# Optimization experiments

Measured on AMD Instinct MI355X. Metric: run time of the kernel, lower is better.

## Reference

```python
import jax, jax.numpy as jnp
import numpy as np

B, L, D = 32, 256, 1024
H = 8
DQ = D // H            # 128, dim_q == dim_k
DS = 64                # dim_s
DM = 256               # dim_mlp_s
DF = 4096              # dim_feedforward
EPS = 1e-5


def _layernorm(x, g, b):
    mu = jnp.mean(x, axis=-1, keepdims=True)
    var = jnp.mean(jnp.square(x - mu), axis=-1, keepdims=True)
    return (x - mu) * jax.lax.rsqrt(var + EPS) * g + b


def setup_inputs() -> dict:
    key = jax.random.key(0)
    ks = jax.random.split(key, 20)
    s = 0.02
    inp = {
        'src': jax.random.normal(ks[0], (B, L, D), jnp.float32),
        'sf': jax.random.normal(ks[1], (B, DS), jnp.float32),
        'atten_mask': jax.random.randint(ks[2], (B, L, L), 0, 2, jnp.int32),
        # per-head projections, stacked over heads (in,out layout)
        'qw': jax.random.normal(ks[3], (H, D, DQ), jnp.float32) * s,
        'qb': jnp.zeros((H, DQ), jnp.float32),
        'kw': jax.random.normal(ks[4], (H, D, DQ), jnp.float32) * s,
        'kb': jnp.zeros((H, DQ), jnp.float32),
        'vw': jax.random.normal(ks[5], (H, D, DQ), jnp.float32) * s,
        'vb': jnp.zeros((H, DQ), jnp.float32),
        # per-head bias MLP: dim_s -> dim_mlp_s -> L*L
        'b1w': jax.random.normal(ks[6], (H, DS, DM), jnp.float32) * s,
        'b1b': jnp.zeros((H, DM), jnp.float32),
        'b2w': jax.random.normal(ks[7], (H, DM, L * L), jnp.float32) * s,
        'b2b': jnp.zeros((H, L * L), jnp.float32),
        # output projection
        'ow': jax.random.normal(ks[8], (H * DQ, D), jnp.float32) * s,
        'ob': jnp.zeros((D,), jnp.float32),
        # layernorms
        'ln1_g': jnp.ones((D,), jnp.float32), 'ln1_b': jnp.zeros((D,), jnp.float32),
        'ln2_g': jnp.ones((D,), jnp.float32), 'ln2_b': jnp.zeros((D,), jnp.float32),
        # feed-forward
        'w1': jax.random.normal(ks[9], (D, DF), jnp.float32) * s,
        'bf1': jnp.zeros((DF,), jnp.float32),
        'w2': jax.random.normal(ks[10], (DF, D), jnp.float32) * s,
        'bf2': jnp.zeros((D,), jnp.float32),
    }
    return inp


def reference(src, sf, atten_mask, qw, qb, kw, kb, vw, vb, b1w, b1b, b2w, b2b,
              ow, ob, ln1_g, ln1_b, ln2_g, ln2_b, w1, bf1, w2, bf2):
    mask = atten_mask.astype(bool)                      # (B,L,L)
    # per-head projections: (H,B,L,DQ)
    q = jnp.einsum('bld,hdq->hblq', src, qw) + qb[:, None, None, :]
    k = jnp.einsum('bld,hdq->hblq', src, kw) + kb[:, None, None, :]
    v = jnp.einsum('bld,hdq->hblq', src, vw) + vb[:, None, None, :]
    scale = q.shape[-1] ** 0.5
    scores = jnp.einsum('hblq,hbmq->hblm', q, k) / scale
    # masked_fill with constant 1e-9 (NOT -inf), as in the original
    scores = jnp.where(mask[None], jnp.float32(1e-9), scores)
    # per-head learned bias from side features, added AFTER softmax
    hid = jax.nn.relu(jnp.einsum('bs,hsm->hbm', sf, b1w) + b1b[:, None, :])
    bias = (jnp.einsum('hbm,hmn->hbn', hid, b2w) + b2b[:, None, :]).reshape(H, B, L, L)
    soft = jax.nn.softmax(scores, axis=-1) + bias
    out = jnp.einsum('hblm,hbmv->hblv', soft, v)        # (H,B,L,DQ)
    # faithful to original: each head's result is indexed [0] -> batch element 0
    head0 = out[:, 0]                                   # (H,L,DQ)
    hidden = jnp.transpose(head0, (1, 0, 2)).reshape(L, H * DQ)
    attn = hidden @ ow + ob                             # (L,D), broadcasts over batch
    x = _layernorm(src + attn[None], ln1_g, ln1_b)      # (B,L,D)
    ffn = jax.nn.relu(x @ w1 + bf1) @ w2 + bf2
    return _layernorm(x + ffn, ln2_g, ln2_b)
```

## Files before the change

kernel.cpp:

```cpp
#include <hip/hip_runtime.h>

typedef unsigned short u16;
typedef short s16x8 __attribute__((ext_vector_type(8)));
typedef u16 u16x4 __attribute__((ext_vector_type(4)));
typedef float f32x4 __attribute__((ext_vector_type(4)));

#define B_ 32
#define L_ 256
#define D_ 1024
#define H_ 8
#define DQ_ 128
#define DS_ 64
#define DM_ 256
#define DF_ 4096

__device__ __forceinline__ u16 f2bf(float f) {
  unsigned u = __float_as_uint(f);
  unsigned r = (u + 0x7FFFu + ((u >> 16) & 1u)) >> 16;
  return (u16)r;
}
__device__ __forceinline__ float bf2f(u16 x) {
  return __uint_as_float(((unsigned)x) << 16);
}

__device__ __forceinline__ f32x4 mfma16(s16x8 a, s16x8 b, f32x4 c) {
  return __builtin_amdgcn_mfma_f32_16x16x32_bf16(a, b, c, 0, 0, 0);
}

#define GLDS16(g, l)                                                        \
  __builtin_amdgcn_global_load_lds(                                         \
      (__attribute__((address_space(1))) const void*)(g),                   \
      (__attribute__((address_space(3))) void*)(l), 16, 0, 0)

__device__ __forceinline__ void tile_tr(const float* __restrict__ ip,
                                        u16* __restrict__ op, int K, int N,
                                        int bx, int by, float (*t)[33], int tid) {
  const int tx = tid & 31, ty = tid >> 5;
  const long n0 = (long)bx * 32, k0 = (long)by * 32;
#pragma unroll
  for (int i = 0; i < 4; ++i)
    t[ty + i * 8][tx] = ip[(k0 + ty + i * 8) * (long)N + n0 + tx];
  __syncthreads();
#pragma unroll
  for (int i = 0; i < 4; ++i)
    op[(n0 + ty + i * 8) * (long)K + k0 + tx] = f2bf(t[tx][ty + i * 8]);
}

__global__ __launch_bounds__(256) void prep(
    const float* __restrict__ qw, const float* __restrict__ kw,
    const float* __restrict__ vw, const float* __restrict__ ow,
    const float* __restrict__ w1, const float* __restrict__ w2,
    const float* __restrict__ src, const float* __restrict__ sf,
    const float* __restrict__ b1w, const float* __restrict__ b1b,
    u16* __restrict__ qwT, u16* __restrict__ kwT, u16* __restrict__ vwT,
    u16* __restrict__ owT, u16* __restrict__ w1T, u16* __restrict__ w2T,
    u16* __restrict__ src0b, float* __restrict__ nzv, int* __restrict__ nzi,
    int* __restrict__ nzcnt) {
  const int b = blockIdx.x;
  const int tid = threadIdx.x;
  __shared__ float t[32][33];
  __shared__ float s_sf[DS_];
  __shared__ int wcnt[4];
  if (b < 3072) {
    const int z = b >> 7, rem = b & 127;
    const int sel = z >> 3, h = z & 7;
    const float* ip = (sel == 0 ? qw : (sel == 1 ? kw : vw)) + (long)h * D_ * DQ_;
    u16* op = (sel == 0 ? qwT : (sel == 1 ? kwT : vwT)) + (long)h * DQ_ * D_;
    tile_tr(ip, op, D_, DQ_, rem & 3, rem >> 2, t, tid);
  } else if (b < 4096) {
    const int rem = b - 3072;
    tile_tr(ow, owT, D_, D_, rem & 31, rem >> 5, t, tid);
  } else if (b < 8192) {
    const int rem = b - 4096;
    tile_tr(w1, w1T, D_, DF_, rem & 127, rem >> 7, t, tid);
  } else if (b < 12288) {
    const int rem = b - 8192;
    tile_tr(w2, w2T, DF_, D_, rem & 31, rem >> 5, t, tid);
  } else if (b < 12544) {
    const int rem = b - 12288;
    const int i = (rem * 256 + tid) * 4;
    float4 v = *(const float4*)(src + i);
    u16x4 o = {f2bf(v.x), f2bf(v.y), f2bf(v.z), f2bf(v.w)};
    *(u16x4*)(src0b + i) = o;
  } else {
    const int h = b - 12544;
    if (tid < DS_) s_sf[tid] = sf[tid];
    __syncthreads();
    float a = b1b[h * DM_ + tid];
    const float* wp = b1w + (long)h * DS_ * DM_ + tid;
#pragma unroll 8
    for (int s = 0; s < DS_; ++s) a += s_sf[s] * wp[s * DM_];
    a = fmaxf(a, 0.f);
    const unsigned long long bal = __ballot(a > 0.f);
    const int lane = tid & 63, wv = tid >> 6;
    const int pc = __popcll(bal);
    if (lane == 0) wcnt[wv] = pc;
    __syncthreads();
    int base = 0;
    for (int i = 0; i < wv; ++i) base += wcnt[i];
    const int pos = base + __popcll(bal & ((1ull << lane) - 1ull));
    if (a > 0.f) { nzv[h * DM_ + pos] = a; nzi[h * DM_ + pos] = tid; }
    if (tid == 255) nzcnt[h] = base + pc;
  }
}

__global__ __launch_bounds__(256) void phase2(
    const float* __restrict__ nzv, const int* __restrict__ nzi,
    const int* __restrict__ nzcnt, const float* __restrict__ b2w,
    const float* __restrict__ b2b, float* __restrict__ biasb,
    const u16* __restrict__ src0b, const u16* __restrict__ qwT,
    const u16* __restrict__ kwT, const u16* __restrict__ vwT,
    const float* __restrict__ qb, const float* __restrict__ kb,
    const float* __restrict__ vb, u16* __restrict__ q0, u16* __restrict__ k0,
    u16* __restrict__ v0T) {
  const int b = blockIdx.x;
  const int tid = threadIdx.x;
  __shared__ float sv[DM_];
  __shared__ int si[DM_];
  __shared__ u16 smA[128 * 32];
  __shared__ u16 smB[128 * 32];
  if (b < 512) {
    const int h = b >> 6;
    const int n0 = (b & 63) << 10;
    const int nnz = nzcnt[h];
    if (tid < DM_) { sv[tid] = nzv[h * DM_ + tid]; si[tid] = nzi[h * DM_ + tid]; }
    __syncthreads();
    const float* wb = b2w + (long)h * DM_ * 65536 + n0 + tid * 4;
    float4 acc = {0.f, 0.f, 0.f, 0.f};
    int j = 0;
    for (; j + 4 <= nnz; j += 4) {
      const float4 a0 = *(const float4*)(wb + (long)si[j] * 65536);
      const float4 a1 = *(const float4*)(wb + (long)si[j + 1] * 65536);
      const float4 a2 = *(const float4*)(wb + (long)si[j + 2] * 65536);
      const float4 a3 = *(const float4*)(wb + (long)si[j + 3] * 65536);
      const float v0 = sv[j], v1 = sv[j + 1], v2 = sv[j + 2], v3 = sv[j + 3];
      acc.x += v0 * a0.x + v1 * a1.x + v2 * a2.x + v3 * a3.x;
      acc.y += v0 * a0.y + v1 * a1.y + v2 * a2.y + v3 * a3.y;
      acc.z += v0 * a0.z + v1 * a1.z + v2 * a2.z + v3 * a3.z;
      acc.w += v0 * a0.w + v1 * a1.w + v2 * a2.w + v3 * a3.w;
    }
    for (; j < nnz; ++j) {
      const float4 a0 = *(const float4*)(wb + (long)si[j] * 65536);
      const float v0 = sv[j];
      acc.x += v0 * a0.x; acc.y += v0 * a0.y; acc.z += v0 * a0.z; acc.w += v0 * a0.w;
    }
    const float4 bb = *(const float4*)(b2b + (long)h * 65536 + n0 + tid * 4);
    float4 o = {acc.x + bb.x, acc.y + bb.y, acc.z + bb.z, acc.w + bb.w};
    *(float4*)(biasb + (long)h * 65536 + n0 + tid * 4) = o;
  } else {
    const int r = b - 512;
    const int z = r >> 1, sel = z >> 3, h = z & 7;
    const long tm = (long)(r & 1) * 128;
    const int K = D_;
    const u16* BT = (sel == 0 ? qwT : (sel == 1 ? kwT : vwT)) + (long)h * DQ_ * D_;
    const float* bias = (sel == 0 ? qb : (sel == 1 ? kb : vb)) + h * DQ_;
    const int lane = tid & 63;
    const int wv = tid >> 6;
    const int wr = wv >> 1, wc = wv & 1;
    const u16* ga = src0b + (tm + (tid >> 2)) * (long)K + (tid & 3) * 8;
    const u16* gb = BT + (long)(tid >> 2) * K + (tid & 3) * 8;
    const long rstep = 64L * K;
    u16* la = &smA[tid * 8];
    u16* lb = &smB[tid * 8];
    f32x4 acc[4][4];
#pragma unroll
    for (int m = 0; m < 4; ++m)
#pragma unroll
      for (int n = 0; n < 4; ++n) acc[m][n] = (f32x4){0.f, 0.f, 0.f, 0.f};
    for (int k0_ = 0; k0_ < K; k0_ += 32) {
      GLDS16(ga + k0_, la);
      GLDS16(ga + rstep + k0_, la + 64 * 32);
      GLDS16(gb + k0_, lb);
      GLDS16(gb + rstep + k0_, lb + 64 * 32);
      __syncthreads();
      s16x8 af[4], bf[4];
      const int ka = (lane >> 4) * 8;
      const int ra = wr * 64 + (lane & 15);
      const int rb = wc * 64 + (lane & 15);
#pragma unroll
      for (int m = 0; m < 4; ++m) af[m] = *(const s16x8*)&smA[(ra + m * 16) * 32 + ka];
#pragma unroll
      for (int n = 0; n < 4; ++n) bf[n] = *(const s16x8*)&smB[(rb + n * 16) * 32 + ka];
#pragma unroll
      for (int m = 0; m < 4; ++m)
#pragma unroll
        for (int n = 0; n < 4; ++n) acc[m][n] = mfma16(af[m], bf[n], acc[m][n]);
      __syncthreads();
    }
    const long crow0 = tm + wr * 64 + ((lane >> 4) * 4);
    const long ccol0 = wc * 64 + (lane & 15);
#pragma unroll
    for (int m = 0; m < 4; ++m) {
#pragma unroll
      for (int n = 0; n < 4; ++n) {
#pragma unroll
        for (int i = 0; i < 4; ++i) {
          const long row = crow0 + m * 16 + i;
          const long col = ccol0 + n * 16;
          const float v = acc[m][n][i] + bias[col];
          if (sel < 2) {
            u16* o = (sel == 0 ? q0 : k0) + (long)h * L_ * DQ_;
            o[row * DQ_ + col] = f2bf(v);
          } else {
            v0T[(long)h * DQ_ * L_ + col * L_ + row] = f2bf(v);
          }
        }
      }
    }
  }
}

__global__ __launch_bounds__(256) void gemm_bt(
    const u16* __restrict__ A, const u16* __restrict__ BT, float* __restrict__ C,
    const float* __restrict__ bias, int K, int ldc) {
  __shared__ u16 smA[128 * 32];
  __shared__ u16 smB[128 * 32];
  const int tid = threadIdx.x;
  const int lane = tid & 63;
  const int wv = tid >> 6;
  const int wr = wv >> 1, wc = wv & 1;
  const long tm = (long)blockIdx.x * 128;
  const long tn = (long)blockIdx.y * 128;

  const u16* ga = A + (tm + (tid >> 2)) * (long)K + (tid & 3) * 8;
  const u16* gb = BT + (tn + (tid >> 2)) * (long)K + (tid & 3) * 8;
  const long rstep = 64L * K;
  u16* la = &smA[tid * 8];
  u16* lb = &smB[tid * 8];

  f32x4 acc[4][4];
#pragma unroll
  for (int m = 0; m < 4; ++m)
#pragma unroll
    for (int n = 0; n < 4; ++n) acc[m][n] = (f32x4){0.f, 0.f, 0.f, 0.f};

  for (int k0 = 0; k0 < K; k0 += 32) {
    GLDS16(ga + k0, la);
    GLDS16(ga + rstep + k0, la + 64 * 32);
    GLDS16(gb + k0, lb);
    GLDS16(gb + rstep + k0, lb + 64 * 32);
    __syncthreads();
    s16x8 af[4], bf[4];
    const int ka = (lane >> 4) * 8;
    const int ra = wr * 64 + (lane & 15);
    const int rb = wc * 64 + (lane & 15);
#pragma unroll
    for (int m = 0; m < 4; ++m) af[m] = *(const s16x8*)&smA[(ra + m * 16) * 32 + ka];
#pragma unroll
    for (int n = 0; n < 4; ++n) bf[n] = *(const s16x8*)&smB[(rb + n * 16) * 32 + ka];
#pragma unroll
    for (int m = 0; m < 4; ++m)
#pragma unroll
      for (int n = 0; n < 4; ++n) acc[m][n] = mfma16(af[m], bf[n], acc[m][n]);
    __syncthreads();
  }

  const long crow0 = tm + wr * 64 + ((lane >> 4) * 4);
  const long ccol0 = tn + wc * 64 + (lane & 15);
#pragma unroll
  for (int m = 0; m < 4; ++m)
#pragma unroll
    for (int n = 0; n < 4; ++n)
#pragma unroll
      for (int i = 0; i < 4; ++i) {
        const long row = crow0 + m * 16 + i;
        const long col = ccol0 + n * 16;
        C[row * (long)ldc + col] = acc[m][n][i] + bias[col];
      }
}

template <int BN, int EPI>
__global__ __launch_bounds__(512, 2) void gemm8p(
    const u16* __restrict__ A, const u16* __restrict__ BT, void* __restrict__ Cv,
    const float* __restrict__ bias, const void* __restrict__ R, int M, int N,
    int K, int ldc) {
  extern __shared__ char lds[];
  constexpr int NR = BN / 64;
  constexpr int NHB = BN / 128;
  constexpr int BUF = 32768 + BN * 128;
  constexpr int WST = (NHB == 2) ? 4 : 2;
  const int tid = threadIdx.x;
  const int lane = tid & 63;
  const int w = tid >> 6;
  const int wr = w >> 2, wc = w & 3;

  const int total = gridDim.x;
  int bid = blockIdx.x;
  int s = ((total & 7) == 0) ? ((bid & 7) * (total >> 3) + (bid >> 3)) : bid;
  const int gn = N / BN;
  const long tm = (long)(s / gn) * 256;
  const long tn = (long)(s % gn) * BN;
  const int NT = K >> 6;

  auto stageA = [&](int half, int t) {
    char* hb = lds + (long)(t & 1) * BUF + half * 16384;
    const u16* g = A + (tm + half * 128) * (long)K + (long)t * 64;
#pragma unroll
    for (int j = 0; j < 2; ++j) {
      const int idx = j * 512 + tid;
      const int r = idx >> 3;
      const int c16 = (idx & 7) ^ (r & 7);
      GLDS16(g + (long)r * K + c16 * 8, hb + idx * 16);
    }
  };
  auto stageB = [&](int half, int t) {
    char* hb = lds + (long)(t & 1) * BUF + 32768 + half * 16384;
    const u16* g = BT + (tn + half * 128) * (long)K + (long)t * 64;
#pragma unroll
    for (int j = 0; j < 2; ++j) {
      const int idx = j * 512 + tid;
      const int r = idx >> 3;
      const int c16 = (idx & 7) ^ (r & 7);
      GLDS16(g + (long)r * K + c16 * 8, hb + idx * 16);
    }
  };

  stageA(0, 0);
  stageA(1, 0);
  stageB(0, 0);
  if (NHB == 2) stageB(1, 0);
  stageB(0, 1);
  if (NHB == 2) stageB(1, 1);
  asm volatile("s_waitcnt vmcnt(%0)" ::"n"(WST) : "memory");
  __builtin_amdgcn_s_barrier();

  f32x4 acc[8][NR];
#pragma unroll
  for (int m = 0; m < 8; ++m)
#pragma unroll
    for (int n = 0; n < NR; ++n) acc[m][n] = (f32x4){0.f, 0.f, 0.f, 0.f};

  const int lk = (lane >> 4) * 16;
  const int lr = lane & 15;

  for (int t = 0; t < NT; ++t) {
    const char* bp = lds + (long)(t & 1) * BUF;
    s16x8 bfr[NR][2];
#pragma unroll
    for (int p = 0; p < 4; ++p) {
      if (p == 0) {
#pragma unroll
        for (int ni = 0; ni < NR; ++ni) {
          const int brow = wc * (BN / 4) + ni * 16 + lr;
#pragma unroll
          for (int ks = 0; ks < 2; ++ks) {
            const int kb = (ks * 64 + lk) ^ ((brow & 7) << 4);
            bfr[ni][ks] = *(const s16x8*)(bp + 32768 + brow * 128 + kb);
          }
        }
      }
      s16x8 afr[2][2];
#pragma unroll
      for (int rI = 0; rI < 2; ++rI) {
        const int arow = wr * 128 + (2 * p + rI) * 16 + lr;
#pragma unroll
        for (int ks = 0; ks < 2; ++ks) {
          const int kb = (ks * 64 + lk) ^ ((arow & 7) << 4);
          afr[rI][ks] = *(const s16x8*)(bp + arow * 128 + kb);
        }
      }
      if (p == 0) {
        if (t + 1 < NT) stageA(0, t + 1);
      } else if (p == 1) {
        if (t + 1 < NT) stageA(1, t + 1);
      } else if (p == 2) {
        if (t + 2 < NT) stageB(0, t + 2);
      } else {
        if (NHB == 2 && t + 2 < NT) stageB(1, t + 2);
      }
      __builtin_amdgcn_s_barrier();
      __builtin_amdgcn_s_setprio(1);
#pragma unroll
      for (int rI = 0; rI < 2; ++rI)
#pragma unroll
        for (int ni = 0; ni < NR; ++ni)
#pragma unroll
          for (int ks = 0; ks < 2; ++ks)
            acc[2 * p + rI][ni] = mfma16(afr[rI][ks], bfr[ni][ks], acc[2 * p + rI][ni]);
      __builtin_amdgcn_s_setprio(0);
      if (p == 3) {
        if (t + 2 < NT) {
          asm volatile("s_waitcnt vmcnt(%0)" ::"n"(WST) : "memory");
        } else if (t + 1 < NT) {
          asm volatile("s_waitcnt vmcnt(0)" ::: "memory");
        }
      }
      __builtin_amdgcn_s_barrier();
    }
  }

  const long crow0 = tm + wr * 128 + ((lane >> 4) * 4);
  const long ccol0 = tn + wc * (BN / 4) + lr;
#pragma unroll
  for (int m = 0; m < 8; ++m) {
#pragma unroll
    for (int n = 0; n < NR; ++n) {
#pragma unroll
      for (int i = 0; i < 4; ++i) {
        const long row = crow0 + m * 16 + i;
        const long col = ccol0 + n * 16;
        const float v = acc[m][n][i] + bias[col];
        if constexpr (EPI == 1) {
          ((u16*)Cv)[row * (long)ldc + col] = f2bf(fmaxf(v, 0.f));
        } else {
          const float r = bf2f(((const u16*)R)[row * (long)ldc + col]);
          ((u16*)Cv)[row * (long)ldc + col] = f2bf(v + r);
        }
      }
    }
  }
}

__global__ __launch_bounds__(64) void attn_kernel(
    const u16* __restrict__ q0, const u16* __restrict__ k0,
    const u16* __restrict__ vT, const float* __restrict__ biasb,
    const int* __restrict__ mask0, u16* __restrict__ hidden) {
  const int lane = threadIdx.x;
  const int h = blockIdx.y;
  const int r0 = blockIdx.x * 16;
  const u16* q = q0 + (long)h * L_ * DQ_;
  const u16* k = k0 + (long)h * L_ * DQ_;
  const u16* v = vT + (long)h * DQ_ * L_;
  const int lg = lane >> 4;
  const int ll = lane & 15;

  s16x8 aq[4];
#pragma unroll
  for (int kk = 0; kk < 4; ++kk)
    aq[kk] = *(const s16x8*)(q + (long)(r0 + ll) * DQ_ + kk * 32 + lg * 8);

  float sc[16][4];
  const float scale = 0.08838834764831845f;
#pragma unroll
  for (int t = 0; t < 16; ++t) {
    f32x4 a = {0.f, 0.f, 0.f, 0.f};
#pragma unroll
    for (int kk = 0; kk < 4; ++kk) {
      s16x8 bf = *(const s16x8*)(k + (long)(t * 16 + ll) * DQ_ + kk * 32 + lg * 8);
      a = mfma16(aq[kk], bf, a);
    }
#pragma unroll
    for (int i = 0; i < 4; ++i) {
      const int row = r0 + lg * 4 + i;
      const int col = t * 16 + ll;
      float s = a[i] * scale;
      if (mask0[row * L_ + col] != 0) s = 1e-9f;
      sc[t][i] = s;
    }
  }
#pragma unroll
  for (int i = 0; i < 4; ++i) {
    float mx = sc[0][i];
#pragma unroll
    for (int t = 1; t < 16; ++t) mx = fmaxf(mx, sc[t][i]);
#pragma unroll
    for (int d = 1; d < 16; d <<= 1) mx = fmaxf(mx, __shfl_xor(mx, d));
    float sum = 0.f;
#pragma unroll
    for (int t = 0; t < 16; ++t) {
      const float e = __expf(sc[t][i] - mx);
      sc[t][i] = e;
      sum += e;
    }
#pragma unroll
    for (int d = 1; d < 16; d <<= 1) sum += __shfl_xor(sum, d);
    const float inv = 1.f / sum;
    const int row = r0 + lg * 4 + i;
#pragma unroll
    for (int t = 0; t < 16; ++t)
      sc[t][i] = sc[t][i] * inv + biasb[(long)h * 65536 + (long)row * 256 + t * 16 + ll];
  }
  __shared__ float sm[16 * 256];
#pragma unroll
  for (int t = 0; t < 16; ++t)
#pragma unroll
    for (int i = 0; i < 4; ++i)
      sm[(lg * 4 + i) * 256 + t * 16 + ll] = sc[t][i];
  __syncthreads();
  s16x8 af[8];
#pragma unroll
  for (int kk = 0; kk < 8; ++kk) {
    const float* ap = &sm[ll * 256 + kk * 32 + lg * 8];
    s16x8 t8;
#pragma unroll
    for (int j = 0; j < 8; ++j) t8[j] = (short)f2bf(ap[j]);
    af[kk] = t8;
  }
#pragma unroll
  for (int n = 0; n < 8; ++n) {
    f32x4 a = {0.f, 0.f, 0.f, 0.f};
#pragma unroll
    for (int kk = 0; kk < 8; ++kk) {
      s16x8 bf = *(const s16x8*)(v + (long)(n * 16 + ll) * 256 + kk * 32 + lg * 8);
      a = mfma16(af[kk], bf, a);
    }
#pragma unroll
    for (int i = 0; i < 4; ++i) {
      const int row = r0 + lg * 4 + i;
      const int col = n * 16 + ll;
      hidden[(long)row * 1024 + h * 128 + col] = f2bf(a[i]);
    }
  }
}

template <int MODE>
__global__ __launch_bounds__(256) void ln_kernel(
    const void* __restrict__ in0v, const float* __restrict__ add1,
    const float* __restrict__ g, const float* __restrict__ bb,
    void* __restrict__ outv) {
  const int tid = threadIdx.x;
  const long row = blockIdx.x;
  float4 v;
  if constexpr (MODE == 0) {
    v = ((const float4*)((const float*)in0v + row * D_))[tid];
    const float4 u = ((const float4*)(add1 + (row & (L_ - 1)) * D_))[tid];
    v.x += u.x; v.y += u.y; v.z += u.z; v.w += u.w;
  } else {
    const uint2 pk = *(const uint2*)((const u16*)in0v + row * D_ + tid * 4);
    v.x = __uint_as_float((pk.x & 0xFFFFu) << 16);
    v.y = __uint_as_float(pk.x & 0xFFFF0000u);
    v.z = __uint_as_float((pk.y & 0xFFFFu) << 16);
    v.w = __uint_as_float(pk.y & 0xFFFF0000u);
  }
  float s = v.x + v.y + v.z + v.w;
  float q = v.x * v.x + v.y * v.y + v.z * v.z + v.w * v.w;
#pragma unroll
  for (int d = 1; d < 64; d <<= 1) { s += __shfl_xor(s, d); q += __shfl_xor(q, d); }
  __shared__ float ss[4], sq[4];
  const int wv = tid >> 6;
  if ((tid & 63) == 0) { ss[wv] = s; sq[wv] = q; }
  __syncthreads();
  s = ss[0] + ss[1] + ss[2] + ss[3];
  q = sq[0] + sq[1] + sq[2] + sq[3];
  const float mu = s * (1.f / D_);
  const float var = q * (1.f / D_) - mu * mu;
  const float rs = rsqrtf(var + 1e-5f);
  const float4 gv = ((const float4*)g)[tid];
  const float4 bv = ((const float4*)bb)[tid];
  float4 o;
  o.x = (v.x - mu) * rs * gv.x + bv.x;
  o.y = (v.y - mu) * rs * gv.y + bv.y;
  o.z = (v.z - mu) * rs * gv.z + bv.z;
  o.w = (v.w - mu) * rs * gv.w + bv.w;
  if constexpr (MODE == 0) {
    uint2 pk;
    pk.x = (unsigned)f2bf(o.x) | ((unsigned)f2bf(o.y) << 16);
    pk.y = (unsigned)f2bf(o.z) | ((unsigned)f2bf(o.w) << 16);
    *(uint2*)((u16*)outv + row * D_ + tid * 4) = pk;
  } else {
    ((float4*)((float*)outv + row * D_))[tid] = o;
  }
}

extern "C" void kernel_launch(void* const* d_in, const int* in_sizes, int n_in,
                              void* d_out, int out_size, void* d_ws, size_t ws_size,
                              hipStream_t stream) {
  (void)in_sizes; (void)n_in; (void)out_size; (void)ws_size;
  const float* src = (const float*)d_in[0];
  const float* sf = (const float*)d_in[1];
  const int* mask = (const int*)d_in[2];
  const float* qw = (const float*)d_in[3];
  const float* qb = (const float*)d_in[4];
  const float* kw = (const float*)d_in[5];
  const float* kb = (const float*)d_in[6];
  const float* vw = (const float*)d_in[7];
  const float* vb = (const float*)d_in[8];
  const float* b1w = (const float*)d_in[9];
  const float* b1b = (const float*)d_in[10];
  const float* b2w = (const float*)d_in[11];
  const float* b2b = (const float*)d_in[12];
  const float* ow = (const float*)d_in[13];
  const float* ob = (const float*)d_in[14];
  const float* ln1g = (const float*)d_in[15];
  const float* ln1b = (const float*)d_in[16];
  const float* ln2g = (const float*)d_in[17];
  const float* ln2b = (const float*)d_in[18];
  const float* w1 = (const float*)d_in[19];
  const float* bf1 = (const float*)d_in[20];
  const float* w2 = (const float*)d_in[21];
  const float* bf2 = (const float*)d_in[22];
  float* out = (float*)d_out;

  char* ws = (char*)d_ws;
  size_t off = 0;
  auto alloc = [&](size_t bytes) {
    void* p = ws + off;
    off += (bytes + 255) & ~(size_t)255;
    return p;
  };
  u16* qwT = (u16*)alloc((size_t)H_ * DQ_ * D_ * 2);
  u16* kwT = (u16*)alloc((size_t)H_ * DQ_ * D_ * 2);
  u16* vwT = (u16*)alloc((size_t)H_ * DQ_ * D_ * 2);
  u16* owT = (u16*)alloc((size_t)D_ * D_ * 2);
  u16* w1T = (u16*)alloc((size_t)DF_ * D_ * 2);
  u16* w2T = (u16*)alloc((size_t)D_ * DF_ * 2);
  u16* src0b = (u16*)alloc((size_t)L_ * D_ * 2);
  u16* q0 = (u16*)alloc((size_t)H_ * L_ * DQ_ * 2);
  u16* k0 = (u16*)alloc((size_t)H_ * L_ * DQ_ * 2);
  u16* v0T = (u16*)alloc((size_t)H_ * DQ_ * L_ * 2);
  float* nzv = (float*)alloc((size_t)H_ * DM_ * 4);
  int* nzi = (int*)alloc((size_t)H_ * DM_ * 4);
  int* nzcnt = (int*)alloc(256);
  float* biasb = (float*)alloc((size_t)H_ * L_ * L_ * 4);
  u16* hidden = (u16*)alloc((size_t)L_ * H_ * DQ_ * 2);
  float* attnvec = (float*)alloc((size_t)L_ * D_ * 4);
  u16* xb = (u16*)alloc((size_t)B_ * L_ * D_ * 2);
  u16* ffnh = (u16*)alloc((size_t)B_ * L_ * DF_ * 2);
  u16* yb = (u16*)alloc((size_t)B_ * L_ * D_ * 2);

  hipFuncSetAttribute((const void*)gemm8p<256, 1>,
                      hipFuncAttributeMaxDynamicSharedMemorySize, 131072);
  hipFuncSetAttribute((const void*)gemm8p<128, 2>,
                      hipFuncAttributeMaxDynamicSharedMemorySize, 98304);

  const dim3 b256(256);
  prep<<<dim3(12552), b256, 0, stream>>>(qw, kw, vw, ow, w1, w2, src, sf, b1w, b1b,
                                         qwT, kwT, vwT, owT, w1T, w2T, src0b, nzv,
                                         nzi, nzcnt);
  phase2<<<dim3(560), b256, 0, stream>>>(nzv, nzi, nzcnt, b2w, b2b, biasb, src0b,
                                         qwT, kwT, vwT, qb, kb, vb, q0, k0, v0T);
  attn_kernel<<<dim3(16, H_), dim3(64), 0, stream>>>(q0, k0, v0T, biasb, mask, hidden);
  gemm_bt<<<dim3(2, 8), b256, 0, stream>>>(hidden, owT, attnvec, ob, D_, D_);
  ln_kernel<0><<<dim3(B_ * L_), b256, 0, stream>>>(src, attnvec, ln1g, ln1b, xb);
  gemm8p<256, 1><<<dim3(512), dim3(512), 131072, stream>>>(
      xb, w1T, ffnh, bf1, nullptr, B_ * L_, DF_, D_, DF_);
  gemm8p<128, 2><<<dim3(256), dim3(512), 98304, stream>>>(
      ffnh, w2T, yb, bf2, xb, B_ * L_, D_, DF_, D_);
  ln_kernel<1><<<dim3(B_ * L_), b256, 0, stream>>>(yb, nullptr, ln2g, ln2b, out);
}
```

Measured before the change: 329.0 us.

## Fuse mid-pipeline stages into cooperative persistent kernels with grid syncs

Replaces the separate phase2, attention, output projection and LN1 launches with one cooperative persistent kernel. It uses an atomic work queue for the bias GEMV and QKV items, then grid-wide syncs between attention, projection and LN1. The FFN2 GEMM and final LayerNorm are likewise fused into one cooperative kernel with a grid sync. This cuts launch overhead and inter-kernel bubbles, at the cost of grid.sync latency, reduced parallelism in some phases (e.g. only 16 blocks for projection), and co-residency requirements for cooperative launch.

```diff
diff --git a/kernel.cpp b/kernel.cpp
--- a/kernel.cpp
+++ b/kernel.cpp
@@ -1,4 +1,7 @@
 #include <hip/hip_runtime.h>
+#include <hip/hip_cooperative_groups.h>
+
+namespace cg = cooperative_groups;
 
 typedef unsigned short u16;
 typedef short s16x8 __attribute__((ext_vector_type(8)));
@@ -55,7 +58,7 @@
     u16* __restrict__ qwT, u16* __restrict__ kwT, u16* __restrict__ vwT,
     u16* __restrict__ owT, u16* __restrict__ w1T, u16* __restrict__ w2T,
     u16* __restrict__ src0b, float* __restrict__ nzv, int* __restrict__ nzi,
-    int* __restrict__ nzcnt) {
+    int* __restrict__ nzcnt, int* __restrict__ qhead) {
   const int b = blockIdx.x;
   const int tid = threadIdx.x;
   __shared__ float t[32][33];
@@ -84,6 +87,7 @@
     *(u16x4*)(src0b + i) = o;
   } else {
     const int h = b - 12544;
+    if (h == 0 && tid == 0) *qhead = 0;
     if (tid < DS_) s_sf[tid] = sf[tid];
     __syncthreads();
     float a = b1b[h * DM_ + tid];
@@ -104,136 +108,35 @@
   }
 }
 
-__global__ __launch_bounds__(256) void phase2(
-    const float* __restrict__ nzv, const int* __restrict__ nzi,
-    const int* __restrict__ nzcnt, const float* __restrict__ b2w,
-    const float* __restrict__ b2b, float* __restrict__ biasb,
-    const u16* __restrict__ src0b, const u16* __restrict__ qwT,
-    const u16* __restrict__ kwT, const u16* __restrict__ vwT,
-    const float* __restrict__ qb, const float* __restrict__ kb,
-    const float* __restrict__ vb, u16* __restrict__ q0, u16* __restrict__ k0,
-    u16* __restrict__ v0T) {
-  const int b = blockIdx.x;
-  const int tid = threadIdx.x;
-  __shared__ float sv[DM_];
-  __shared__ int si[DM_];
-  __shared__ u16 smA[128 * 32];
-  __shared__ u16 smB[128 * 32];
-  if (b < 512) {
-    const int h = b >> 6;
-    const int n0 = (b & 63) << 10;
-    const int nnz = nzcnt[h];
-    if (tid < DM_) { sv[tid] = nzv[h * DM_ + tid]; si[tid] = nzi[h * DM_ + tid]; }
-    __syncthreads();
-    const float* wb = b2w + (long)h * DM_ * 65536 + n0 + tid * 4;
-    float4 acc = {0.f, 0.f, 0.f, 0.f};
-    int j = 0;
-    for (; j + 4 <= nnz; j += 4) {
-      const float4 a0 = *(const float4*)(wb + (long)si[j] * 65536);
-      const float4 a1 = *(const float4*)(wb + (long)si[j + 1] * 65536);
-      const float4 a2 = *(const float4*)(wb + (long)si[j + 2] * 65536);
-      const float4 a3 = *(const float4*)(wb + (long)si[j + 3] * 65536);
-      const float v0 = sv[j], v1 = sv[j + 1], v2 = sv[j + 2], v3 = sv[j + 3];
-      acc.x += v0 * a0.x + v1 * a1.x + v2 * a2.x + v3 * a3.x;
-      acc.y += v0 * a0.y + v1 * a1.y + v2 * a2.y + v3 * a3.y;
-      acc.z += v0 * a0.z + v1 * a1.z + v2 * a2.z + v3 * a3.z;
-      acc.w += v0 * a0.w + v1 * a1.w + v2 * a2.w + v3 * a3.w;
-    }
-    for (; j < nnz; ++j) {
-      const float4 a0 = *(const float4*)(wb + (long)si[j] * 65536);
-      const float v0 = sv[j];
-      acc.x += v0 * a0.x; acc.y += v0 * a0.y; acc.z += v0 * a0.z; acc.w += v0 * a0.w;
-    }
-    const float4 bb = *(const float4*)(b2b + (long)h * 65536 + n0 + tid * 4);
-    float4 o = {acc.x + bb.x, acc.y + bb.y, acc.z + bb.z, acc.w + bb.w};
-    *(float4*)(biasb + (long)h * 65536 + n0 + tid * 4) = o;
-  } else {
-    const int r = b - 512;
-    const int z = r >> 1, sel = z >> 3, h = z & 7;
-    const long tm = (long)(r & 1) * 128;
-    const int K = D_;
-    const u16* BT = (sel == 0 ? qwT : (sel == 1 ? kwT : vwT)) + (long)h * DQ_ * D_;
-    const float* bias = (sel == 0 ? qb : (sel == 1 ? kb : vb)) + h * DQ_;
-    const int lane = tid & 63;
-    const int wv = tid >> 6;
-    const int wr = wv >> 1, wc = wv & 1;
-    const u16* ga = src0b + (tm + (tid >> 2)) * (long)K + (tid & 3) * 8;
-    const u16* gb = BT + (long)(tid >> 2) * K + (tid & 3) * 8;
-    const long rstep = 64L * K;
-    u16* la = &smA[tid * 8];
-    u16* lb = &smB[tid * 8];
-    f32x4 acc[4][4];
-#pragma unroll
-    for (int m = 0; m < 4; ++m)
-#pragma unroll
-      for (int n = 0; n < 4; ++n) acc[m][n] = (f32x4){0.f, 0.f, 0.f, 0.f};
-    for (int k0_ = 0; k0_ < K; k0_ += 32) {
-      GLDS16(ga + k0_, la);
-      GLDS16(ga + rstep + k0_, la + 64 * 32);
-      GLDS16(gb + k0_, lb);
-      GLDS16(gb + rstep + k0_, lb + 64 * 32);
-      __syncthreads();
-      s16x8 af[4], bf[4];
-      const int ka = (lane >> 4) * 8;
-      const int ra = wr * 64 + (lane & 15);
-      const int rb = wc * 64 + (lane & 15);
-#pragma unroll
-      for (int m = 0; m < 4; ++m) af[m] = *(const s16x8*)&smA[(ra + m * 16) * 32 + ka];
-#pragma unroll
-      for (int n = 0; n < 4; ++n) bf[n] = *(const s16x8*)&smB[(rb + n * 16) * 32 + ka];
-#pragma unroll
-      for (int m = 0; m < 4; ++m)
-#pragma unroll
-        for (int n = 0; n < 4; ++n) acc[m][n] = mfma16(af[m], bf[n], acc[m][n]);
-      __syncthreads();
-    }
-    const long crow0 = tm + wr * 64 + ((lane >> 4) * 4);
-    const long ccol0 = wc * 64 + (lane & 15);
-#pragma unroll
-    for (int m = 0; m < 4; ++m) {
-#pragma unroll
-      for (int n = 0; n < 4; ++n) {
-#pragma unroll
-        for (int i = 0; i < 4; ++i) {
-          const long row = crow0 + m * 16 + i;
-          const long col = ccol0 + n * 16;
-          const float v = acc[m][n][i] + bias[col];
-          if (sel < 2) {
-            u16* o = (sel == 0 ? q0 : k0) + (long)h * L_ * DQ_;
-            o[row * DQ_ + col] = f2bf(v);
-          } else {
-            v0T[(long)h * DQ_ * L_ + col * L_ + row] = f2bf(v);
-          }
-        }
-      }
-    }
-  }
-}
-
-__global__ __launch_bounds__(256) void gemm_bt(
-    const u16* __restrict__ A, const u16* __restrict__ BT, float* __restrict__ C,
-    const float* __restrict__ bias, int K, int ldc) {
-  __shared__ u16 smA[128 * 32];
-  __shared__ u16 smB[128 * 32];
+struct MidArgs {
+  const float* nzv; const int* nzi; const int* nzcnt;
+  const float* b2w; const float* b2b; float* biasb;
+  const u16* src0b; const u16* qwT; const u16* kwT; const u16* vwT;
+  const float* qb; const float* kb; const float* vb;
+  u16* q0; u16* k0; u16* v0T;
+  const int* mask; u16* hidden;
+  const u16* owT; const float* ob; float* attnvec;
+  const float* src; const float* ln1g; const float* ln1b; u16* xb;
+  int* qhead;
+};
+
+__device__ __forceinline__ void g128_core(const u16* __restrict__ A,
+                                          const u16* __restrict__ BT, int K,
+                                          u16* smA, u16* smB,
+                                          f32x4 (&acc)[4][4]) {
   const int tid = threadIdx.x;
   const int lane = tid & 63;
   const int wv = tid >> 6;
   const int wr = wv >> 1, wc = wv & 1;
-  const long tm = (long)blockIdx.x * 128;
-  const long tn = (long)blockIdx.y * 128;
-
-  const u16* ga = A + (tm + (tid >> 2)) * (long)K + (tid & 3) * 8;
-  const u16* gb = BT + (tn + (tid >> 2)) * (long)K + (tid & 3) * 8;
+  const u16* ga = A + (long)(tid >> 2) * K + (tid & 3) * 8;
+  const u16* gb = BT + (long)(tid >> 2) * K + (tid & 3) * 8;
   const long rstep = 64L * K;
   u16* la = &smA[tid * 8];
   u16* lb = &smB[tid * 8];
-
-  f32x4 acc[4][4];
 #pragma unroll
   for (int m = 0; m < 4; ++m)
 #pragma unroll
     for (int n = 0; n < 4; ++n) acc[m][n] = (f32x4){0.f, 0.f, 0.f, 0.f};
-
   for (int k0 = 0; k0 < K; k0 += 32) {
     GLDS16(ga + k0, la);
     GLDS16(ga + rstep + k0, la + 64 * 32);
@@ -254,9 +157,55 @@
       for (int n = 0; n < 4; ++n) acc[m][n] = mfma16(af[m], bf[n], acc[m][n]);
     __syncthreads();
   }
-
+}
+
+__device__ __forceinline__ void gemv_item(int item, const MidArgs& a,
+                                          float* sv, int* si) {
+  const int tid = threadIdx.x;
+  const int h = item >> 6;
+  const int n0 = (item & 63) << 10;
+  const int nnz = a.nzcnt[h];
+  sv[tid] = a.nzv[h * DM_ + tid];
+  si[tid] = a.nzi[h * DM_ + tid];
+  __syncthreads();
+  const float* wb = a.b2w + (long)h * DM_ * 65536 + n0 + tid * 4;
+  float4 acc = {0.f, 0.f, 0.f, 0.f};
+  int j = 0;
+  for (; j + 4 <= nnz; j += 4) {
+    const float4 a0 = *(const float4*)(wb + (long)si[j] * 65536);
+    const float4 a1 = *(const float4*)(wb + (long)si[j + 1] * 65536);
+    const float4 a2 = *(const float4*)(wb + (long)si[j + 2] * 65536);
+    const float4 a3 = *(const float4*)(wb + (long)si[j + 3] * 65536);
+    const float v0 = sv[j], v1 = sv[j + 1], v2 = sv[j + 2], v3 = sv[j + 3];
+    acc.x += v0 * a0.x + v1 * a1.x + v2 * a2.x + v3 * a3.x;
+    acc.y += v0 * a0.y + v1 * a1.y + v2 * a2.y + v3 * a3.y;
+    acc.z += v0 * a0.z + v1 * a1.z + v2 * a2.z + v3 * a3.z;
+    acc.w += v0 * a0.w + v1 * a1.w + v2 * a2.w + v3 * a3.w;
+  }
+  for (; j < nnz; ++j) {
+    const float4 a0 = *(const float4*)(wb + (long)si[j] * 65536);
+    const float v0 = sv[j];
+    acc.x += v0 * a0.x; acc.y += v0 * a0.y; acc.z += v0 * a0.z; acc.w += v0 * a0.w;
+  }
+  const float4 bb = *(const float4*)(a.b2b + (long)h * 65536 + n0 + tid * 4);
+  float4 o = {acc.x + bb.x, acc.y + bb.y, acc.z + bb.z, acc.w + bb.w};
+  *(float4*)(a.biasb + (long)h * 65536 + n0 + tid * 4) = o;
+}
+
+__device__ __forceinline__ void qkv_item(int r, const MidArgs& a, u16* smA,
+                                         u16* smB) {
+  const int tid = threadIdx.x;
+  const int z = r >> 1, sel = z >> 3, h = z & 7;
+  const long tm = (long)(r & 1) * 128;
+  const u16* BT = (sel == 0 ? a.qwT : (sel == 1 ? a.kwT : a.vwT)) + (long)h * DQ_ * D_;
+  const float* bias = (sel == 0 ? a.qb : (sel == 1 ? a.kb : a.vb)) + h * DQ_;
+  f32x4 acc[4][4];
+  g128_core(a.src0b + tm * D_, BT, D_, smA, smB, acc);
+  const int lane = tid & 63;
+  const int wv = tid >> 6;
+  const int wr = wv >> 1, wc = wv & 1;
   const long crow0 = tm + wr * 64 + ((lane >> 4) * 4);
-  const long ccol0 = tn + wc * 64 + (lane & 15);
+  const long ccol0 = wc * 64 + (lane & 15);
 #pragma unroll
   for (int m = 0; m < 4; ++m)
 #pragma unroll
@@ -265,25 +214,203 @@
       for (int i = 0; i < 4; ++i) {
         const long row = crow0 + m * 16 + i;
         const long col = ccol0 + n * 16;
-        C[row * (long)ldc + col] = acc[m][n][i] + bias[col];
-      }
-}
-
-template <int BN, int EPI>
-__global__ __launch_bounds__(512, 2) void gemm8p(
-    const u16* __restrict__ A, const u16* __restrict__ BT, void* __restrict__ Cv,
-    const float* __restrict__ bias, const void* __restrict__ R, int M, int N,
-    int K, int ldc) {
+        const float v = acc[m][n][i] + bias[col];
+        if (sel < 2) {
+          u16* o = (sel == 0 ? a.q0 : a.k0) + (long)h * L_ * DQ_;
+          o[row * DQ_ + col] = f2bf(v);
+        } else {
+          a.v0T[(long)h * DQ_ * L_ + col * L_ + row] = f2bf(v);
+        }
+      }
+}
+
+__device__ void attn_item(int item, const MidArgs& a, float* sm) {
+  const int tid = threadIdx.x;
+  const int h = item >> 4;
+  const int r0 = (item & 15) << 4;
+  const u16* q = a.q0 + (long)h * L_ * DQ_;
+  const u16* k = a.k0 + (long)h * L_ * DQ_;
+  const u16* v = a.v0T + (long)h * DQ_ * L_;
+  const int lg = (tid >> 4) & 3;
+  const int ll = tid & 15;
+  float sc[16][4];
+  if (tid < 64) {
+    s16x8 aq[4];
+#pragma unroll
+    for (int kk = 0; kk < 4; ++kk)
+      aq[kk] = *(const s16x8*)(q + (long)(r0 + ll) * DQ_ + kk * 32 + lg * 8);
+    const float scale = 0.08838834764831845f;
+#pragma unroll
+    for (int t = 0; t < 16; ++t) {
+      f32x4 acc = {0.f, 0.f, 0.f, 0.f};
+#pragma unroll
+      for (int kk = 0; kk < 4; ++kk) {
+        s16x8 bf = *(const s16x8*)(k + (long)(t * 16 + ll) * DQ_ + kk * 32 + lg * 8);
+        acc = mfma16(aq[kk], bf, acc);
+      }
+#pragma unroll
+      for (int i = 0; i < 4; ++i) {
+        const int row = r0 + lg * 4 + i;
+        const int col = t * 16 + ll;
+        float s = acc[i] * scale;
+        if (a.mask[row * L_ + col] != 0) s = 1e-9f;
+        sc[t][i] = s;
+      }
+    }
+#pragma unroll
+    for (int i = 0; i < 4; ++i) {
+      float mx = sc[0][i];
+#pragma unroll
+      for (int t = 1; t < 16; ++t) mx = fmaxf(mx, sc[t][i]);
+#pragma unroll
+      for (int d = 1; d < 16; d <<= 1) mx = fmaxf(mx, __shfl_xor(mx, d));
+      float sum = 0.f;
+#pragma unroll
+      for (int t = 0; t < 16; ++t) {
+        const float e = __expf(sc[t][i] - mx);
+        sc[t][i] = e;
+        sum += e;
+      }
+#pragma unroll
+      for (int d = 1; d < 16; d <<= 1) sum += __shfl_xor(sum, d);
+      const float inv = 1.f / sum;
+      const int row = r0 + lg * 4 + i;
+#pragma unroll
+      for (int t = 0; t < 16; ++t)
+        sc[t][i] = sc[t][i] * inv + a.biasb[(long)h * 65536 + (long)row * 256 + t * 16 + ll];
+    }
+#pragma unroll
+    for (int t = 0; t < 16; ++t)
+#pragma unroll
+      for (int i = 0; i < 4; ++i)
+        sm[(lg * 4 + i) * 256 + t * 16 + ll] = sc[t][i];
+  }
+  __syncthreads();
+  if (tid < 64) {
+    s16x8 af[8];
+#pragma unroll
+    for (int kk = 0; kk < 8; ++kk) {
+      const float* ap = &sm[ll * 256 + kk * 32 + lg * 8];
+      s16x8 t8;
+#pragma unroll
+      for (int j = 0; j < 8; ++j) t8[j] = (short)f2bf(ap[j]);
+      af[kk] = t8;
+    }
+#pragma unroll
+    for (int n = 0; n < 8; ++n) {
+      f32x4 acc = {0.f, 0.f, 0.f, 0.f};
+#pragma unroll
+      for (int kk = 0; kk < 8; ++kk) {
+        s16x8 bf = *(const s16x8*)(v + (long)(n * 16 + ll) * 256 + kk * 32 + lg * 8);
+        acc = mfma16(af[kk], bf, acc);
+      }
+#pragma unroll
+      for (int i = 0; i < 4; ++i) {
+        const int row = r0 + lg * 4 + i;
+        const int col = n * 16 + ll;
+        a.hidden[(long)row * 1024 + h * 128 + col] = f2bf(acc[i]);
+      }
+    }
+  }
+}
+
+__device__ __forceinline__ void proj_item(int item, const MidArgs& a, u16* smA,
+                                          u16* smB) {
+  const int tid = threadIdx.x;
+  const long tm = (long)(item >> 3) * 128;
+  const long tn = (long)(item & 7) * 128;
+  f32x4 acc[4][4];
+  g128_core(a.hidden + tm * D_, a.owT + tn * D_, D_, smA, smB, acc);
+  const int lane = tid & 63;
+  const int wv = tid >> 6;
+  const int wr = wv >> 1, wc = wv & 1;
+  const long crow0 = tm + wr * 64 + ((lane >> 4) * 4);
+  const long ccol0 = tn + wc * 64 + (lane & 15);
+#pragma unroll
+  for (int m = 0; m < 4; ++m)
+#pragma unroll
+    for (int n = 0; n < 4; ++n)
+#pragma unroll
+      for (int i = 0; i < 4; ++i) {
+        const long row = crow0 + m * 16 + i;
+        const long col = ccol0 + n * 16;
+        a.attnvec[row * (long)D_ + col] = acc[m][n][i] + a.ob[col];
+      }
+}
+
+__device__ __forceinline__ void ln1_rows(const MidArgs& a) {
+  const int tid = threadIdx.x;
+  __shared__ float ss[4], sq[4];
+  for (int r = 0; r < 32; ++r) {
+    const long row = (long)blockIdx.x * 32 + r;
+    float4 v = ((const float4*)(a.src + row * D_))[tid];
+    const float4 u = ((const float4*)(a.attnvec + (row & (L_ - 1)) * D_))[tid];
+    v.x += u.x; v.y += u.y; v.z += u.z; v.w += u.w;
+    float s = v.x + v.y + v.z + v.w;
+    float q = v.x * v.x + v.y * v.y + v.z * v.z + v.w * v.w;
+#pragma unroll
+    for (int d = 1; d < 64; d <<= 1) { s += __shfl_xor(s, d); q += __shfl_xor(q, d); }
+    const int wv = tid >> 6;
+    if ((tid & 63) == 0) { ss[wv] = s; sq[wv] = q; }
+    __syncthreads();
+    s = ss[0] + ss[1] + ss[2] + ss[3];
+    q = sq[0] + sq[1] + sq[2] + sq[3];
+    const float mu = s * (1.f / D_);
+    const float var = q * (1.f / D_) - mu * mu;
+    const float rs = rsqrtf(var + 1e-5f);
+    const float4 gv = ((const float4*)a.ln1g)[tid];
+    const float4 bv = ((const float4*)a.ln1b)[tid];
+    float4 o;
+    o.x = (v.x - mu) * rs * gv.x + bv.x;
+    o.y = (v.y - mu) * rs * gv.y + bv.y;
+    o.z = (v.z - mu) * rs * gv.z + bv.z;
+    o.w = (v.w - mu) * rs * gv.w + bv.w;
+    uint2 pk;
+    pk.x = (unsigned)f2bf(o.x) | ((unsigned)f2bf(o.y) << 16);
+    pk.y = (unsigned)f2bf(o.z) | ((unsigned)f2bf(o.w) << 16);
+    *(uint2*)(a.xb + row * D_ + tid * 4) = pk;
+    __syncthreads();
+  }
+}
+
+__global__ __launch_bounds__(256) void mid_kernel(MidArgs a) {
+  __shared__ u16 smA[128 * 32];
+  __shared__ u16 smB[128 * 32];
+  __shared__ float sv[DM_];
+  __shared__ int si[DM_];
+  __shared__ float smf[16 * 256];
+  __shared__ int s_item;
+  const int tid = threadIdx.x;
+  cg::grid_group grid = cg::this_grid();
+  for (;;) {
+    if (tid == 0)
+      s_item = __hip_atomic_fetch_add(a.qhead, 1, __ATOMIC_RELAXED,
+                                      __HIP_MEMORY_SCOPE_AGENT);
+    __syncthreads();
+    const int item = s_item;
+    __syncthreads();
+    if (item >= 560) break;
+    if (item < 512) gemv_item(item, a, sv, si);
+    else qkv_item(item - 512, a, smA, smB);
+  }
+  grid.sync();
+  if (blockIdx.x < 128) attn_item(blockIdx.x, a, smf);
+  grid.sync();
+  if (blockIdx.x < 16) proj_item(blockIdx.x, a, smA, smB);
+  grid.sync();
+  ln1_rows(a);
+}
+
+__global__ __launch_bounds__(512, 2) void gemm8p_ffn1(
+    const u16* __restrict__ A, const u16* __restrict__ BT, u16* __restrict__ C,
+    const float* __restrict__ bias) {
   extern __shared__ char lds[];
-  constexpr int NR = BN / 64;
-  constexpr int NHB = BN / 128;
-  constexpr int BUF = 32768 + BN * 128;
-  constexpr int WST = (NHB == 2) ? 4 : 2;
+  constexpr int BN = 256, NR = 4, BUF = 32768 + BN * 128, WST = 4;
+  const int K = D_, N = DF_, ldc = DF_;
   const int tid = threadIdx.x;
   const int lane = tid & 63;
   const int w = tid >> 6;
   const int wr = w >> 2, wc = w & 3;
-
   const int total = gridDim.x;
   int bid = blockIdx.x;
   int s = ((total & 7) == 0) ? ((bid & 7) * (total >> 3) + (bid >> 3)) : bid;
@@ -315,12 +442,8 @@
     }
   };
 
-  stageA(0, 0);
-  stageA(1, 0);
-  stageB(0, 0);
-  if (NHB == 2) stageB(1, 0);
-  stageB(0, 1);
-  if (NHB == 2) stageB(1, 1);
+  stageA(0, 0); stageA(1, 0); stageB(0, 0); stageB(1, 0);
+  stageB(0, 1); stageB(1, 1);
   asm volatile("s_waitcnt vmcnt(%0)" ::"n"(WST) : "memory");
   __builtin_amdgcn_s_barrier();
 
@@ -359,15 +482,10 @@
           afr[rI][ks] = *(const s16x8*)(bp + arow * 128 + kb);
         }
       }
-      if (p == 0) {
-        if (t + 1 < NT) stageA(0, t + 1);
-      } else if (p == 1) {
-        if (t + 1 < NT) stageA(1, t + 1);
-      } else if (p == 2) {
-        if (t + 2 < NT) stageB(0, t + 2);
-      } else {
-        if (NHB == 2 && t + 2 < NT) stageB(1, t + 2);
-      }
+      if (p == 0) { if (t + 1 < NT) stageA(0, t + 1); }
+      else if (p == 1) { if (t + 1 < NT) stageA(1, t + 1); }
+      else if (p == 2) { if (t + 2 < NT) stageB(0, t + 2); }
+      else { if (t + 2 < NT) stageB(1, t + 2); }
       __builtin_amdgcn_s_barrier();
       __builtin_amdgcn_s_setprio(1);
 #pragma unroll
@@ -392,163 +510,176 @@
   const long crow0 = tm + wr * 128 + ((lane >> 4) * 4);
   const long ccol0 = tn + wc * (BN / 4) + lr;
 #pragma unroll
-  for (int m = 0; m < 8; ++m) {
-#pragma unroll
-    for (int n = 0; n < NR; ++n) {
+  for (int m = 0; m < 8; ++m)
+#pragma unroll
+    for (int n = 0; n < NR; ++n)
 #pragma unroll
       for (int i = 0; i < 4; ++i) {
         const long row = crow0 + m * 16 + i;
         const long col = ccol0 + n * 16;
         const float v = acc[m][n][i] + bias[col];
-        if constexpr (EPI == 1) {
-          ((u16*)Cv)[row * (long)ldc + col] = f2bf(fmaxf(v, 0.f));
-        } else {
-          const float r = bf2f(((const u16*)R)[row * (long)ldc + col]);
-          ((u16*)Cv)[row * (long)ldc + col] = f2bf(v + r);
+        C[row * (long)ldc + col] = f2bf(fmaxf(v, 0.f));
+      }
+}
+
+__global__ __launch_bounds__(512, 2) void ffn2_ln2(
+    const u16* __restrict__ A, const u16* __restrict__ BT, u16* __restrict__ yb,
+    const float* __restrict__ bias, const u16* __restrict__ Rb,
+    const float* __restrict__ g2, const float* __restrict__ bb2,
+    float* __restrict__ out) {
+  extern __shared__ char lds[];
+  constexpr int BN = 128, NR = 2, BUF = 32768 + BN * 128, WST = 2;
+  const int K = DF_, N = D_, ldc = D_;
+  const int tid = threadIdx.x;
+  const int lane = tid & 63;
+  const int w = tid >> 6;
+  const int wr = w >> 2, wc = w & 3;
+  const int total = gridDim.x;
+  int bid = blockIdx.x;
+  int s = ((total & 7) == 0) ? ((bid & 7) * (total >> 3) + (bid >> 3)) : bid;
+  const int gn = N / BN;
+  const long tm = (long)(s / gn) * 256;
+  const long tn = (long)(s % gn) * BN;
+  const int NT = K >> 6;
+
+  auto stageA = [&](int half, int t) {
+    char* hb = lds + (long)(t & 1) * BUF + half * 16384;
+    const u16* g = A + (tm + half * 128) * (long)K + (long)t * 64;
+#pragma unroll
+    for (int j = 0; j < 2; ++j) {
+      const int idx = j * 512 + tid;
+      const int r = idx >> 3;
+      const int c16 = (idx & 7) ^ (r & 7);
+      GLDS16(g + (long)r * K + c16 * 8, hb + idx * 16);
+    }
+  };
+  auto stageB = [&](int t) {
+    char* hb = lds + (long)(t & 1) * BUF + 32768;
+    const u16* g = BT + tn * (long)K + (long)t * 64;
+#pragma unroll
+    for (int j = 0; j < 2; ++j) {
+      const int idx = j * 512 + tid;
+      const int r = idx >> 3;
+      const int c16 = (idx & 7) ^ (r & 7);
+      GLDS16(g + (long)r * K + c16 * 8, hb + idx * 16);
+    }
+  };
+
+  stageA(0, 0); stageA(1, 0); stageB(0); stageB(1);
+  asm volatile("s_waitcnt vmcnt(%0)" ::"n"(WST) : "memory");
+  __builtin_amdgcn_s_barrier();
+
+  f32x4 acc[8][NR];
+#pragma unroll
+  for (int m = 0; m < 8; ++m)
+#pragma unroll
+    for (int n = 0; n < NR; ++n) acc[m][n] = (f32x4){0.f, 0.f, 0.f, 0.f};
+
+  const int lk = (lane >> 4) * 16;
+  const int lr = lane & 15;
+
+  for (int t = 0; t < NT; ++t) {
+    const char* bp = lds + (long)(t & 1) * BUF;
+    s16x8 bfr[NR][2];
+#pragma unroll
+    for (int p = 0; p < 4; ++p) {
+      if (p == 0) {
+#pragma unroll
+        for (int ni = 0; ni < NR; ++ni) {
+          const int brow = wc * (BN / 4) + ni * 16 + lr;
+#pragma unroll
+          for (int ks = 0; ks < 2; ++ks) {
+            const int kb = (ks * 64 + lk) ^ ((brow & 7) << 4);
+            bfr[ni][ks] = *(const s16x8*)(bp + 32768 + brow * 128 + kb);
+          }
         }
       }
-    }
-  }
-}
-
-__global__ __launch_bounds__(64) void attn_kernel(
-    const u16* __restrict__ q0, const u16* __restrict__ k0,
-    const u16* __restrict__ vT, const float* __restrict__ biasb,
-    const int* __restrict__ mask0, u16* __restrict__ hidden) {
-  const int lane = threadIdx.x;
-  const int h = blockIdx.y;
-  const int r0 = blockIdx.x * 16;
-  const u16* q = q0 + (long)h * L_ * DQ_;
-  const u16* k = k0 + (long)h * L_ * DQ_;
-  const u16* v = vT + (long)h * DQ_ * L_;
-  const int lg = lane >> 4;
-  const int ll = lane & 15;
-
-  s16x8 aq[4];
-#pragma unroll
-  for (int kk = 0; kk < 4; ++kk)
-    aq[kk] = *(const s16x8*)(q + (long)(r0 + ll) * DQ_ + kk * 32 + lg * 8);
-
-  float sc[16][4];
-  const float scale = 0.08838834764831845f;
-#pragma unroll
-  for (int t = 0; t < 16; ++t) {
-    f32x4 a = {0.f, 0.f, 0.f, 0.f};
-#pragma unroll
-    for (int kk = 0; kk < 4; ++kk) {
-      s16x8 bf = *(const s16x8*)(k + (long)(t * 16 + ll) * DQ_ + kk * 32 + lg * 8);
-      a = mfma16(aq[kk], bf, a);
-    }
-#pragma unroll
-    for (int i = 0; i < 4; ++i) {
-      const int row = r0 + lg * 4 + i;
-      const int col = t * 16 + ll;
-      float s = a[i] * scale;
-      if (mask0[row * L_ + col] != 0) s = 1e-9f;
-      sc[t][i] = s;
-    }
-  }
-#pragma unroll
-  for (int i = 0; i < 4; ++i) {
-    float mx = sc[0][i];
-#pragma unroll
-    for (int t = 1; t < 16; ++t) mx = fmaxf(mx, sc[t][i]);
-#pragma unroll
-    for (int d = 1; d < 16; d <<= 1) mx = fmaxf(mx, __shfl_xor(mx, d));
-    float sum = 0.f;
-#pragma unroll
-    for (int t = 0; t < 16; ++t) {
-      const float e = __expf(sc[t][i] - mx);
-      sc[t][i] = e;
-      sum += e;
-    }
-#pragma unroll
-    for (int d = 1; d < 16; d <<= 1) sum += __shfl_xor(sum, d);
-    const float inv = 1.f / sum;
-    const int row = r0 + lg * 4 + i;
-#pragma unroll
-    for (int t = 0; t < 16; ++t)
-      sc[t][i] = sc[t][i] * inv + biasb[(long)h * 65536 + (long)row * 256 + t * 16 + ll];
-  }
-  __shared__ float sm[16 * 256];
-#pragma unroll
-  for (int t = 0; t < 16; ++t)
-#pragma unroll
-    for (int i = 0; i < 4; ++i)
-      sm[(lg * 4 + i) * 256 + t * 16 + ll] = sc[t][i];
-  __syncthreads();
-  s16x8 af[8];
-#pragma unroll
-  for (int kk = 0; kk < 8; ++kk) {
-    const float* ap = &sm[ll * 256 + kk * 32 + lg * 8];
-    s16x8 t8;
-#pragma unroll
-    for (int j = 0; j < 8; ++j) t8[j] = (short)f2bf(ap[j]);
-    af[kk] = t8;
-  }
-#pragma unroll
-  for (int n = 0; n < 8; ++n) {
-    f32x4 a = {0.f, 0.f, 0.f, 0.f};
-#pragma unroll
-    for (int kk = 0; kk < 8; ++kk) {
-      s16x8 bf = *(const s16x8*)(v + (long)(n * 16 + ll) * 256 + kk * 32 + lg * 8);
-      a = mfma16(af[kk], bf, a);
-    }
-#pragma unroll
-    for (int i = 0; i < 4; ++i) {
-      const int row = r0 + lg * 4 + i;
-      const int col = n * 16 + ll;
-      hidden[(long)row * 1024 + h * 128 + col] = f2bf(a[i]);
-    }
-  }
-}
-
-template <int MODE>
-__global__ __launch_bounds__(256) void ln_kernel(
-    const void* __restrict__ in0v, const float* __restrict__ add1,
-    const float* __restrict__ g, const float* __restrict__ bb,
-    void* __restrict__ outv) {
-  const int tid = threadIdx.x;
-  const long row = blockIdx.x;
-  float4 v;
-  if constexpr (MODE == 0) {
-    v = ((const float4*)((const float*)in0v + row * D_))[tid];
-    const float4 u = ((const float4*)(add1 + (row & (L_ - 1)) * D_))[tid];
-    v.x += u.x; v.y += u.y; v.z += u.z; v.w += u.w;
-  } else {
-    const uint2 pk = *(const uint2*)((const u16*)in0v + row * D_ + tid * 4);
+      s16x8 afr[2][2];
+#pragma unroll
+      for (int rI = 0; rI < 2; ++rI) {
+        const int arow = wr * 128 + (2 * p + rI) * 16 + lr;
+#pragma unroll
+        for (int ks = 0; ks < 2; ++ks) {
+          const int kb = (ks * 64 + lk) ^ ((arow & 7) << 4);
+          afr[rI][ks] = *(const s16x8*)(bp + arow * 128 + kb);
+        }
+      }
+      if (p == 0) { if (t + 1 < NT) stageA(0, t + 1); }
+      else if (p == 1) { if (t + 1 < NT) stageA(1, t + 1); }
+      else if (p == 2) { if (t + 2 < NT) stageB(t + 2); }
+      __builtin_amdgcn_s_barrier();
+      __builtin_amdgcn_s_setprio(1);
+#pragma unroll
+      for (int rI = 0; rI < 2; ++rI)
+#pragma unroll
+        for (int ni = 0; ni < NR; ++ni)
+#pragma unroll
+          for (int ks = 0; ks < 2; ++ks)
+            acc[2 * p + rI][ni] = mfma16(afr[rI][ks], bfr[ni][ks], acc[2 * p + rI][ni]);
+      __builtin_amdgcn_s_setprio(0);
+      if (p == 3) {
+        if (t + 2 < NT) {
+          asm volatile("s_waitcnt vmcnt(%0)" ::"n"(WST) : "memory");
+        } else if (t + 1 < NT) {
+          asm volatile("s_waitcnt vmcnt(0)" ::: "memory");
+        }
+      }
+      __builtin_amdgcn_s_barrier();
+    }
+  }
+
+  {
+    const long crow0 = tm + wr * 128 + ((lane >> 4) * 4);
+    const long ccol0 = tn + wc * (BN / 4) + lr;
+#pragma unroll
+    for (int m = 0; m < 8; ++m)
+#pragma unroll
+      for (int n = 0; n < NR; ++n)
+#pragma unroll
+        for (int i = 0; i < 4; ++i) {
+          const long row = crow0 + m * 16 + i;
+          const long col = ccol0 + n * 16;
+          const float v = acc[m][n][i] + bias[col];
+          const float r = bf2f(Rb[row * (long)ldc + col]);
+          yb[row * (long)ldc + col] = f2bf(v + r);
+        }
+  }
+
+  cg::this_grid().sync();
+
+  float* ssq = (float*)lds;
+  const int tsub = tid & 255;
+  const int grp = tid >> 8;
+  const int wvg = (tid >> 6) & 3;
+  for (int it = 0; it < 16; ++it) {
+    const long row = (long)blockIdx.x * 32 + it * 2 + grp;
+    const uint2 pk = *(const uint2*)(yb + row * D_ + tsub * 4);
+    float4 v;
     v.x = __uint_as_float((pk.x & 0xFFFFu) << 16);
     v.y = __uint_as_float(pk.x & 0xFFFF0000u);
     v.z = __uint_as_float((pk.y & 0xFFFFu) << 16);
     v.w = __uint_as_float(pk.y & 0xFFFF0000u);
-  }
-  float s = v.x + v.y + v.z + v.w;
-  float q = v.x * v.x + v.y * v.y + v.z * v.z + v.w * v.w;
-#pragma unroll
-  for (int d = 1; d < 64; d <<= 1) { s += __shfl_xor(s, d); q += __shfl_xor(q, d); }
-  __shared__ float ss[4], sq[4];
-  const int wv = tid >> 6;
-  if ((tid & 63) == 0) { ss[wv] = s; sq[wv] = q; }
-  __syncthreads();
-  s = ss[0] + ss[1] + ss[2] + ss[3];
-  q = sq[0] + sq[1] + sq[2] + sq[3];
-  const float mu = s * (1.f / D_);
-  const float var = q * (1.f / D_) - mu * mu;
-  const float rs = rsqrtf(var + 1e-5f);
-  const float4 gv = ((const float4*)g)[tid];
-  const float4 bv = ((const float4*)bb)[tid];
-  float4 o;
-  o.x = (v.x - mu) * rs * gv.x + bv.x;
-  o.y = (v.y - mu) * rs * gv.y + bv.y;
-  o.z = (v.z - mu) * rs * gv.z + bv.z;
-  o.w = (v.w - mu) * rs * gv.w + bv.w;
-  if constexpr (MODE == 0) {
-    uint2 pk;
-    pk.x = (unsigned)f2bf(o.x) | ((unsigned)f2bf(o.y) << 16);
-    pk.y = (unsigned)f2bf(o.z) | ((unsigned)f2bf(o.w) << 16);
-    *(uint2*)((u16*)outv + row * D_ + tid * 4) = pk;
-  } else {
-    ((float4*)((float*)outv + row * D_))[tid] = o;
+    float sm = v.x + v.y + v.z + v.w;
+    float qm = v.x * v.x + v.y * v.y + v.z * v.z + v.w * v.w;
+#pragma unroll
+    for (int d = 1; d < 64; d <<= 1) { sm += __shfl_xor(sm, d); qm += __shfl_xor(qm, d); }
+    if ((tid & 63) == 0) { ssq[grp * 4 + wvg] = sm; ssq[8 + grp * 4 + wvg] = qm; }
+    __syncthreads();
+    sm = ssq[grp * 4 + 0] + ssq[grp * 4 + 1] + ssq[grp * 4 + 2] + ssq[grp * 4 + 3];
+    qm = ssq[8 + grp * 4 + 0] + ssq[8 + grp * 4 + 1] + ssq[8 + grp * 4 + 2] +
+         ssq[8 + grp * 4 + 3];
+    const float mu = sm * (1.f / D_);
+    const float var = qm * (1.f / D_) - mu * mu;
+    const float rs = rsqrtf(var + 1e-5f);
+    const float4 gv = ((const float4*)g2)[tsub];
+    const float4 bv = ((const float4*)bb2)[tsub];
+    float4 o;
+    o.x = (v.x - mu) * rs * gv.x + bv.x;
+    o.y = (v.y - mu) * rs * gv.y + bv.y;
+    o.z = (v.z - mu) * rs * gv.z + bv.z;
+    o.w = (v.w - mu) * rs * gv.w + bv.w;
+    ((float4*)(out + row * D_))[tsub] = o;
+    __syncthreads();
   }
 }
 
@@ -607,24 +738,37 @@
   u16* xb = (u16*)alloc((size_t)B_ * L_ * D_ * 2);
   u16* ffnh = (u16*)alloc((size_t)B_ * L_ * DF_ * 2);
   u16* yb = (u16*)alloc((size_t)B_ * L_ * D_ * 2);
-
-  hipFuncSetAttribute((const void*)gemm8p<256, 1>,
+  int* qhead = (int*)alloc(256);
+
+  hipFuncSetAttribute((const void*)gemm8p_ffn1,
                       hipFuncAttributeMaxDynamicSharedMemorySize, 131072);
-  hipFuncSetAttribute((const void*)gemm8p<128, 2>,
+  hipFuncSetAttribute((const void*)ffn2_ln2,
                       hipFuncAttributeMaxDynamicSharedMemorySize, 98304);
 
-  const dim3 b256(256);
-  prep<<<dim3(12552), b256, 0, stream>>>(qw, kw, vw, ow, w1, w2, src, sf, b1w, b1b,
-                                         qwT, kwT, vwT, owT, w1T, w2T, src0b, nzv,
-                                         nzi, nzcnt);
-  phase2<<<dim3(560), b256, 0, stream>>>(nzv, nzi, nzcnt, b2w, b2b, biasb, src0b,
-                                         qwT, kwT, vwT, qb, kb, vb, q0, k0, v0T);
-  attn_kernel<<<dim3(16, H_), dim3(64), 0, stream>>>(q0, k0, v0T, biasb, mask, hidden);
-  gemm_bt<<<dim3(2, 8), b256, 0, stream>>>(hidden, owT, attnvec, ob, D_, D_);
-  ln_kernel<0><<<dim3(B_ * L_), b256, 0, stream>>>(src, attnvec, ln1g, ln1b, xb);
-  gemm8p<256, 1><<<dim3(512), dim3(512), 131072, stream>>>(
-      xb, w1T, ffnh, bf1, nullptr, B_ * L_, DF_, D_, DF_);
-  gemm8p<128, 2><<<dim3(256), dim3(512), 98304, stream>>>(
-      ffnh, w2T, yb, bf2, xb, B_ * L_, D_, DF_, D_);
-  ln_kernel<1><<<dim3(B_ * L_), b256, 0, stream>>>(yb, nullptr, ln2g, ln2b, out);
-}
+  prep<<<dim3(12552), dim3(256), 0, stream>>>(
+      qw, kw, vw, ow, w1, w2, src, sf, b1w, b1b, qwT, kwT, vwT, owT, w1T, w2T,
+      src0b, nzv, nzi, nzcnt, qhead);
+
+  MidArgs ma;
+  ma.nzv = nzv; ma.nzi = nzi; ma.nzcnt = nzcnt;
+  ma.b2w = b2w; ma.b2b = b2b; ma.biasb = biasb;
+  ma.src0b = src0b; ma.qwT = qwT; ma.kwT = kwT; ma.vwT = vwT;
+  ma.qb = qb; ma.kb = kb; ma.vb = vb;
+  ma.q0 = q0; ma.k0 = k0; ma.v0T = v0T;
+  ma.mask = mask; ma.hidden = hidden;
+  ma.owT = owT; ma.ob = ob; ma.attnvec = attnvec;
+  ma.src = src; ma.ln1g = ln1g; ma.ln1b = ln1b; ma.xb = xb;
+  ma.qhead = qhead;
+  void* kpm[] = {&ma};
+  hipLaunchCooperativeKernel((void*)mid_kernel, dim3(256), dim3(256), kpm, 0,
+                             stream);
+
+  gemm8p_ffn1<<<dim3(512), dim3(512), 131072, stream>>>(xb, w1T, ffnh, bf1);
+
+  const u16* aP = ffnh; const u16* btP = w2T; u16* ybP = yb;
+  const float* biP = bf2; const u16* rP = xb;
+  const float* gP = ln2g; const float* bbP = ln2b; float* oP = out;
+  void* kp2[] = {&aP, &btP, &ybP, &biP, &rP, &gP, &bbP, &oP};
+  hipLaunchCooperativeKernel((void*)ffn2_ln2, dim3(256), dim3(512), kp2, 98304,
+                             stream);
+}
```

Measured after the change: 472.8 us. 1.44x slower.
